# Optimization experiments

Hardware: AMD Instinct MI355X
Metric: run time of the kernel (lower is better)

Reference implementation:

```python
import jax, jax.numpy as jnp
import numpy as np

NUM_GROUPS = 32
EPS = 1e-6

def group_norm(x, gamma, beta):
    B, C, H, W = x.shape
    g = x.reshape(B, NUM_GROUPS, C // NUM_GROUPS, H, W)
    mean = g.mean(axis=(2, 3, 4), keepdims=True)
    var = g.var(axis=(2, 3, 4), keepdims=True)
    g = (g - mean) * jax.lax.rsqrt(var + EPS)
    x = g.reshape(B, C, H, W)
    return x * gamma[None, :, None, None] + beta[None, :, None, None]

def conv1x1(x, w, b):
    # x: [B,C,H,W], w: [Cout,Cin], b: [Cout]
    return jnp.einsum('bchw,oc->bohw', x, w) + b[None, :, None, None]

def setup_inputs() -> dict:
    key = jax.random.key(0)
    ks = jax.random.split(key, 11)
    B, C, H, W = 8, 512, 64, 64
    s = 1.0 / np.sqrt(C)
    return {
        'x': jax.random.normal(ks[0], (B, C, H, W), jnp.float32),
        'gn_w': jnp.ones((C,), jnp.float32),
        'gn_b': jnp.zeros((C,), jnp.float32),
        'q_w': jax.random.normal(ks[1], (C, C), jnp.float32) * s,
        'q_b': jnp.zeros((C,), jnp.float32),
        'k_w': jax.random.normal(ks[2], (C, C), jnp.float32) * s,
        'k_b': jnp.zeros((C,), jnp.float32),
        'v_w': jax.random.normal(ks[3], (C, C), jnp.float32) * s,
        'v_b': jnp.zeros((C,), jnp.float32),
        'proj_w': jax.random.normal(ks[4], (C, C), jnp.float32) * s,
        'proj_b': jnp.zeros((C,), jnp.float32),
    }

def reference(x, gn_w, gn_b, q_w, q_b, k_w, k_b, v_w, v_b, proj_w, proj_b):
    B, C, H, W = x.shape
    h = group_norm(x, gn_w, gn_b)
    q = conv1x1(h, q_w, q_b).reshape(B, C, H * W)  # [B,C,N]
    k = conv1x1(h, k_w, k_b).reshape(B, C, H * W)
    v = conv1x1(h, v_w, v_b).reshape(B, C, H * W)
    # scores: [B, N(query), N(key)]
    w = jnp.einsum('bcn,bcm->bnm', q, k) * (C ** -0.5)
    w = jax.nn.softmax(w, axis=2)
    # out: [B, C, N]
    h = jnp.einsum('bnm,bcm->bcn', w, v).reshape(B, C, H, W)
    return x + conv1x1(h, proj_w, proj_b)
```

## Files before the change

### kernel.cpp

```cpp
#include <hip/hip_runtime.h>
#include <hip/hip_bf16.h>
#include <hip/hip_fp16.h>
#include <stdint.h>


#define C_DIM 512
#define N_DIM 4096
#define CN (512 * 4096)
#define BATCH 8

typedef _Float16 h8 __attribute__((ext_vector_type(8)));
typedef _Float16 h4 __attribute__((ext_vector_type(4)));
typedef float f4 __attribute__((ext_vector_type(4)));

__device__ __forceinline__ void gload16(const void* g, void* l) {
  __builtin_amdgcn_global_load_lds((const __attribute__((address_space(1))) void*)g,
                                   (__attribute__((address_space(3))) void*)l, 16, 0, 0);
}

__device__ __forceinline__ void gemm_core(const _Float16* __restrict__ At, int lda,
                                          const _Float16* __restrict__ Bt, int ldb,
                                          int ksteps, _Float16* lsA, _Float16* lsB,
                                          f4 acc[4][4]) {
  const int t = threadIdx.x, w = t >> 6, lane = t & 63;
  const int rr = lane >> 2, kof = (lane & 3) * 8;
  const _Float16* gA0 = At + (size_t)((w * 2 + 0) * 16 + rr) * lda + kof;
  const _Float16* gA1 = At + (size_t)((w * 2 + 1) * 16 + rr) * lda + kof;
  const _Float16* gB0 = Bt + (size_t)((w * 2 + 0) * 16 + rr) * ldb + kof;
  const _Float16* gB1 = Bt + (size_t)((w * 2 + 1) * 16 + rr) * ldb + kof;
  _Float16* lA0 = lsA + (w * 2 + 0) * 512;
  _Float16* lA1 = lsA + (w * 2 + 1) * 512;
  _Float16* lB0 = lsB + (w * 2 + 0) * 512;
  _Float16* lB1 = lsB + (w * 2 + 1) * 512;
  const int wm = w >> 1, wn = w & 1;
  const int fr = lane & 15, fk = (lane >> 4) * 8;
  for (int ks = 0; ks < ksteps; ++ks) {
    gload16(gA0, lA0);
    gload16(gA1, lA1);
    gload16(gB0, lB0);
    gload16(gB1, lB1);
    __syncthreads();
    h8 af[4], bf[4];
#pragma unroll
    for (int i = 0; i < 4; ++i)
      af[i] = *(const h8*)&lsA[(wm * 64 + i * 16 + fr) * 32 + fk];
#pragma unroll
    for (int j = 0; j < 4; ++j)
      bf[j] = *(const h8*)&lsB[(wn * 64 + j * 16 + fr) * 32 + fk];
#pragma unroll
    for (int i = 0; i < 4; ++i)
#pragma unroll
      for (int j = 0; j < 4; ++j)
        acc[i][j] = __builtin_amdgcn_mfma_f32_16x16x32_f16(af[i], bf[j], acc[i][j], 0, 0, 0);
    __syncthreads();
    gA0 += 32; gA1 += 32; gB0 += 32; gB1 += 32;
  }
}

__device__ __forceinline__ void epi_f16_direct(f4 acc[4][4], _Float16* lsOut,
                                               _Float16* out, int ldo,
                                               const float* bias_tile, float scale) {
  const int t = threadIdx.x, lane = t & 63, w = t >> 6, wm = w >> 1, wn = w & 1;
  const int cr = lane >> 4, cc = lane & 15;
#pragma unroll
  for (int i = 0; i < 4; ++i) {
    const int r0 = wm * 64 + i * 16 + cr * 4;
    float b0 = 0.f, b1 = 0.f, b2 = 0.f, b3 = 0.f;
    if (bias_tile) { b0 = bias_tile[r0]; b1 = bias_tile[r0 + 1];
                     b2 = bias_tile[r0 + 2]; b3 = bias_tile[r0 + 3]; }
#pragma unroll
    for (int j = 0; j < 4; ++j) {
      const int cl = wn * 64 + j * 16 + cc;
      lsOut[(r0 + 0) * 136 + cl] = (_Float16)(acc[i][j].x * scale + b0);
      lsOut[(r0 + 1) * 136 + cl] = (_Float16)(acc[i][j].y * scale + b1);
      lsOut[(r0 + 2) * 136 + cl] = (_Float16)(acc[i][j].z * scale + b2);
      lsOut[(r0 + 3) * 136 + cl] = (_Float16)(acc[i][j].w * scale + b3);
    }
  }
  __syncthreads();
  const int row = t >> 1, co = (t & 1) * 64;
#pragma unroll
  for (int s = 0; s < 8; ++s)
    *(uint4*)(out + (size_t)row * ldo + co + s * 8) =
        *(const uint4*)&lsOut[row * 136 + co + s * 8];
}

__device__ __forceinline__ void epi_f16_trans(f4 acc[4][4], _Float16* lsOut,
                                              _Float16* outT, int ldo,
                                              const float* bias_tile) {
  const int t = threadIdx.x, lane = t & 63, w = t >> 6, wm = w >> 1, wn = w & 1;
  const int cr = lane >> 4, cc = lane & 15;
#pragma unroll
  for (int i = 0; i < 4; ++i) {
    const int r0 = wm * 64 + i * 16 + cr * 4;
    const float b0 = bias_tile[r0], b1 = bias_tile[r0 + 1];
    const float b2 = bias_tile[r0 + 2], b3 = bias_tile[r0 + 3];
#pragma unroll
    for (int j = 0; j < 4; ++j) {
      const int cl = wn * 64 + j * 16 + cc;
      h4 v = {(_Float16)(acc[i][j].x + b0), (_Float16)(acc[i][j].y + b1),
              (_Float16)(acc[i][j].z + b2), (_Float16)(acc[i][j].w + b3)};
      *(h4*)&lsOut[cl * 136 + r0] = v;
    }
  }
  __syncthreads();
  const int row = t >> 1, co = (t & 1) * 64;
#pragma unroll
  for (int s = 0; s < 8; ++s)
    *(uint4*)(outT + (size_t)row * ldo + co + s * 8) =
        *(const uint4*)&lsOut[row * 136 + co + s * 8];
}

__device__ __forceinline__ void epi_f32_direct(f4 acc[4][4], float* out, int ldo,
                                               const float* bias_tile,
                                               const float* resid) {
  const int t = threadIdx.x, lane = t & 63, w = t >> 6, wm = w >> 1, wn = w & 1;
  const int cr = lane >> 4, cc = lane & 15;
#pragma unroll
  for (int i = 0; i < 4; ++i) {
    const int r0 = wm * 64 + i * 16 + cr * 4;
#pragma unroll
    for (int r = 0; r < 4; ++r) {
      const int row = r0 + r;
      const float bv = bias_tile ? bias_tile[row] : 0.f;
#pragma unroll
      for (int j = 0; j < 4; ++j) {
        const int col = wn * 64 + j * 16 + cc;
        float v = acc[i][j][r] + bv;
        if (resid) v += resid[(size_t)row * ldo + col];
        out[(size_t)row * ldo + col] = v;
      }
    }
  }
}

__global__ __launch_bounds__(256) void k_wcvt(const float* __restrict__ w0,
                                              const float* __restrict__ w1,
                                              const float* __restrict__ w2,
                                              const float* __restrict__ w3,
                                              _Float16* __restrict__ out) {
  const int z = blockIdx.y;
  const float* src = z == 0 ? w0 : z == 1 ? w1 : z == 2 ? w2 : w3;
  _Float16* dst = out + (size_t)z * (C_DIM * C_DIM);
  const int idx = (blockIdx.x * 256 + threadIdx.x) * 4;
  f4 v = *(const f4*)(src + idx);
  h4 o = {(_Float16)v.x, (_Float16)v.y, (_Float16)v.z, (_Float16)v.w};
  *(h4*)(dst + idx) = o;
}

__global__ __launch_bounds__(256) void k_gnstats(const float* __restrict__ x,
                                                 float* __restrict__ stats) {
  const int bg = blockIdx.x;
  const f4* x4 = (const f4*)(x + (size_t)bg * (16 * N_DIM));
  const int t = threadIdx.x;
  float s = 0.f, ss = 0.f;
#pragma unroll 4
  for (int i = 0; i < 64; ++i) {
    f4 v = x4[t + i * 256];
    s += v.x + v.y + v.z + v.w;
    ss += v.x * v.x + v.y * v.y + v.z * v.z + v.w * v.w;
  }
  __shared__ float reds[4], redq[4];
  for (int off = 32; off; off >>= 1) {
    s += __shfl_down(s, off);
    ss += __shfl_down(ss, off);
  }
  if ((t & 63) == 0) { reds[t >> 6] = s; redq[t >> 6] = ss; }
  __syncthreads();
  if (t == 0) {
    s = reds[0] + reds[1] + reds[2] + reds[3];
    ss = redq[0] + redq[1] + redq[2] + redq[3];
    const float mean = s * (1.f / (16 * N_DIM));
    const float var = ss * (1.f / (16 * N_DIM)) - mean * mean;
    stats[bg * 2] = mean;
    stats[bg * 2 + 1] = rsqrtf(var + 1e-6f);
  }
}

__global__ __launch_bounds__(256) void k_gnapply(const float* __restrict__ x,
                                                 const float* __restrict__ gw,
                                                 const float* __restrict__ gb,
                                                 const float* __restrict__ stats,
                                                 _Float16* __restrict__ Ht) {
  __shared__ _Float16 lsT[64 * 72];
  const int n0 = blockIdx.x * 64, c0 = blockIdx.y * 64, b = blockIdx.z;
  const int t = threadIdx.x, rc = t >> 2, qc = t & 3;
  const int c = c0 + rc, g = c >> 4;
  const float mean = stats[(b * 32 + g) * 2], rstd = stats[(b * 32 + g) * 2 + 1];
  const float sc = gw[c] * rstd, of = gb[c] - mean * sc;
  const float* xr = x + ((size_t)b * C_DIM + c) * N_DIM + n0;
#pragma unroll
  for (int q = 0; q < 4; ++q) {
    const int f4i = qc + q * 4;
    f4 v = *(const f4*)(xr + f4i * 4);
    const int nl = f4i * 4;
    lsT[(nl + 0) * 72 + rc] = (_Float16)(v.x * sc + of);
    lsT[(nl + 1) * 72 + rc] = (_Float16)(v.y * sc + of);
    lsT[(nl + 2) * 72 + rc] = (_Float16)(v.z * sc + of);
    lsT[(nl + 3) * 72 + rc] = (_Float16)(v.w * sc + of);
  }
  __syncthreads();
  const int j = t >> 2, ch = (t & 3) * 16;
  _Float16* dst = Ht + ((size_t)b * N_DIM + n0 + j) * C_DIM + c0 + ch;
  *(uint4*)dst = *(const uint4*)&lsT[j * 72 + ch];
  *(uint4*)(dst + 8) = *(const uint4*)&lsT[j * 72 + ch + 8];
}

__global__ __launch_bounds__(256) void k_qkv(const _Float16* __restrict__ Wh,
                                             const float* __restrict__ bq,
                                             const float* __restrict__ bk,
                                             const float* __restrict__ bv,
                                             const _Float16* __restrict__ Ht,
                                             _Float16* __restrict__ Qt,
                                             _Float16* __restrict__ Kt,
                                             _Float16* __restrict__ V) {
  __shared__ _Float16 smem[128 * 136];
  const int z = blockIdx.z, b = z / 3, which = z - b * 3;
  const _Float16* A = Wh + (size_t)which * (C_DIM * C_DIM);
  const float* bias = which == 0 ? bq : which == 1 ? bk : bv;
  const int n0 = blockIdx.x * 128, m0 = blockIdx.y * 128;
  f4 acc[4][4] = {};
  gemm_core(A + (size_t)m0 * C_DIM, C_DIM,
            Ht + (size_t)b * CN + (size_t)n0 * C_DIM, C_DIM, 16,
            smem, smem + 4096, acc);
  if (which == 2) {
    epi_f16_direct(acc, smem, V + (size_t)b * CN + (size_t)m0 * N_DIM + n0, N_DIM,
                   bias + m0, 1.f);
  } else {
    _Float16* outT = (which == 0 ? Qt : Kt) + (size_t)b * CN + (size_t)n0 * C_DIM + m0;
    epi_f16_trans(acc, smem, outT, C_DIM, bias + m0);
  }
}

__global__ __launch_bounds__(256) void k_qk(const _Float16* __restrict__ Qt,
                                            const _Float16* __restrict__ Kt,
                                            _Float16* __restrict__ S) {
  __shared__ _Float16 smem[128 * 136];
  const int m0 = blockIdx.x * 128, n0 = blockIdx.y * 128;
  f4 acc[4][4] = {};
  gemm_core(Qt + (size_t)n0 * C_DIM, C_DIM, Kt + (size_t)m0 * C_DIM, C_DIM, 16,
            smem, smem + 4096, acc);
  epi_f16_direct(acc, smem, S + (size_t)n0 * N_DIM + m0, N_DIM, nullptr,
                 0.04419417382415922f);
}

__global__ __launch_bounds__(256) void k_softmax(_Float16* __restrict__ S) {
  _Float16* row = S + (size_t)blockIdx.x * N_DIM;
  const int t = threadIdx.x, lane = t & 63, w = t >> 6;
  _Float16 v[16];
  *(uint4*)&v[0] = *(const uint4*)(row + t * 16);
  *(uint4*)&v[8] = *(const uint4*)(row + t * 16 + 8);
  float f[16], mx = -1e30f;
#pragma unroll
  for (int u = 0; u < 16; ++u) { f[u] = (float)v[u]; mx = fmaxf(mx, f[u]); }
  __shared__ float red[8];
  for (int off = 32; off; off >>= 1) mx = fmaxf(mx, __shfl_down(mx, off));
  if (lane == 0) red[w] = mx;
  __syncthreads();
  mx = fmaxf(fmaxf(red[0], red[1]), fmaxf(red[2], red[3]));
  float sum = 0.f;
#pragma unroll
  for (int u = 0; u < 16; ++u) { f[u] = __expf(f[u] - mx); sum += f[u]; }
  for (int off = 32; off; off >>= 1) sum += __shfl_down(sum, off);
  if (lane == 0) red[4 + w] = sum;
  __syncthreads();
  const float inv = 1.f / (red[4] + red[5] + red[6] + red[7]);
#pragma unroll
  for (int u = 0; u < 16; ++u) v[u] = (_Float16)(f[u] * inv);
  *(uint4*)(row + t * 16) = *(const uint4*)&v[0];
  *(uint4*)(row + t * 16 + 8) = *(const uint4*)&v[8];
}

__global__ __launch_bounds__(256) void k_pv(const _Float16* __restrict__ P,
                                            const _Float16* __restrict__ V,
                                            float* __restrict__ Pp) {
  __shared__ _Float16 smem[2 * 4096];
  const int c0 = blockIdx.x * 128, n0 = blockIdx.y * 128, kz = blockIdx.z;
  f4 acc[4][4] = {};
  gemm_core(P + (size_t)n0 * N_DIM + kz * 1024, N_DIM,
            V + (size_t)c0 * N_DIM + kz * 1024, N_DIM, 32,
            smem, smem + 4096, acc);
  epi_f32_direct(acc, Pp + (size_t)kz * CN + (size_t)n0 * C_DIM + c0, C_DIM,
                 nullptr, nullptr);
}

__global__ __launch_bounds__(256) void k_pvred(const float* __restrict__ Pp,
                                               _Float16* __restrict__ ATTt) {
  const int idx = (blockIdx.x * 256 + threadIdx.x) * 8;
  float a[8];
#pragma unroll
  for (int u = 0; u < 8; ++u) a[u] = 0.f;
#pragma unroll
  for (int kz = 0; kz < 4; ++kz) {
    f4 p0 = *(const f4*)(Pp + (size_t)kz * CN + idx);
    f4 p1 = *(const f4*)(Pp + (size_t)kz * CN + idx + 4);
    a[0] += p0.x; a[1] += p0.y; a[2] += p0.z; a[3] += p0.w;
    a[4] += p1.x; a[5] += p1.y; a[6] += p1.z; a[7] += p1.w;
  }
  h8 o = {(_Float16)a[0], (_Float16)a[1], (_Float16)a[2], (_Float16)a[3],
          (_Float16)a[4], (_Float16)a[5], (_Float16)a[6], (_Float16)a[7]};
  *(h8*)(ATTt + idx) = o;
}

__global__ __launch_bounds__(256) void k_proj(const _Float16* __restrict__ Whp,
                                              const float* __restrict__ bp,
                                              const _Float16* __restrict__ ATTt,
                                              const float* __restrict__ x,
                                              float* __restrict__ out) {
  __shared__ _Float16 smem[2 * 4096];
  const int b = blockIdx.z, n0 = blockIdx.x * 128, m0 = blockIdx.y * 128;
  f4 acc[4][4] = {};
  gemm_core(Whp + (size_t)m0 * C_DIM, C_DIM,
            ATTt + (size_t)b * CN + (size_t)n0 * C_DIM, C_DIM, 16,
            smem, smem + 4096, acc);
  const size_t off = (size_t)b * CN + (size_t)m0 * N_DIM + n0;
  epi_f32_direct(acc, out + off, N_DIM, bp + m0, x + off);
}

extern "C" void kernel_launch(void* const* d_in, const int* in_sizes, int n_in,
                              void* d_out, int out_size, void* d_ws, size_t ws_size,
                              hipStream_t stream) {
  const float* x = (const float*)d_in[0];
  const float* gn_w = (const float*)d_in[1];
  const float* gn_b = (const float*)d_in[2];
  const float* q_w = (const float*)d_in[3];
  const float* q_b = (const float*)d_in[4];
  const float* k_w = (const float*)d_in[5];
  const float* k_b = (const float*)d_in[6];
  const float* v_w = (const float*)d_in[7];
  const float* v_b = (const float*)d_in[8];
  const float* p_w = (const float*)d_in[9];
  const float* p_b = (const float*)d_in[10];
  float* out = (float*)d_out;

  const size_t MB = 1024ull * 1024ull;
  if (ws_size < 164ull * MB) return;
  char* ws = (char*)d_ws;
  _Float16* Wh    = (_Float16*)(ws + 0);
  float*    stats = (float*)(ws + 2 * MB);
  _Float16* Ht    = (_Float16*)(ws + 4 * MB);
  _Float16* Qt    = (_Float16*)(ws + 36 * MB);
  _Float16* Kt    = (_Float16*)(ws + 68 * MB);
  _Float16* V     = (_Float16*)(ws + 100 * MB);
  float*    Pp    = (float*)(ws + 132 * MB);
  _Float16* S     = Ht;
  _Float16* ATTt  = Qt;

  k_wcvt<<<dim3(256, 4), 256, 0, stream>>>(q_w, k_w, v_w, p_w, Wh);
  k_gnstats<<<dim3(256), 256, 0, stream>>>(x, stats);
  k_gnapply<<<dim3(64, 8, 8), 256, 0, stream>>>(x, gn_w, gn_b, stats, Ht);
  k_qkv<<<dim3(32, 4, 24), 256, 0, stream>>>(Wh, q_b, k_b, v_b, Ht, Qt, Kt, V);
  for (int b = 0; b < BATCH; ++b) {
    k_qk<<<dim3(32, 32), 256, 0, stream>>>(Qt + (size_t)b * CN, Kt + (size_t)b * CN, S);
    k_softmax<<<dim3(4096), 256, 0, stream>>>(S);
    k_pv<<<dim3(4, 32, 4), 256, 0, stream>>>(S, V + (size_t)b * CN, Pp);
    k_pvred<<<dim3(1024), 256, 0, stream>>>(Pp, ATTt + (size_t)b * CN);
  }
  k_proj<<<dim3(32, 4, 8), 256, 0, stream>>>(Wh + 3 * C_DIM * C_DIM, p_b, ATTt, x, out);
}
```

Baseline: 987.8 us.

## Batch attention over several images per launch and drop split-K PV reduction

```diff
diff --git a/kernel.cpp b/kernel.cpp
--- a/kernel.cpp
+++ b/kernel.cpp
@@ -7,6 +7,7 @@
 #define C_DIM 512
 #define N_DIM 4096
 #define CN (512 * 4096)
+#define NN ((size_t)4096 * 4096)
 #define BATCH 8
 
 typedef _Float16 h8 __attribute__((ext_vector_type(8)));
@@ -236,16 +237,17 @@
                                             const _Float16* __restrict__ Kt,
                                             _Float16* __restrict__ S) {
   __shared__ _Float16 smem[128 * 136];
-  const int m0 = blockIdx.x * 128, n0 = blockIdx.y * 128;
+  const int m0 = blockIdx.x * 128, n0 = blockIdx.y * 128, bz = blockIdx.z;
   f4 acc[4][4] = {};
-  gemm_core(Qt + (size_t)n0 * C_DIM, C_DIM, Kt + (size_t)m0 * C_DIM, C_DIM, 16,
+  gemm_core(Qt + (size_t)bz * CN + (size_t)n0 * C_DIM, C_DIM,
+            Kt + (size_t)bz * CN + (size_t)m0 * C_DIM, C_DIM, 16,
             smem, smem + 4096, acc);
-  epi_f16_direct(acc, smem, S + (size_t)n0 * N_DIM + m0, N_DIM, nullptr,
-                 0.04419417382415922f);
+  epi_f16_direct(acc, smem, S + (size_t)bz * NN + (size_t)n0 * N_DIM + m0, N_DIM,
+                 nullptr, 0.04419417382415922f);
 }
 
 __global__ __launch_bounds__(256) void k_softmax(_Float16* __restrict__ S) {
-  _Float16* row = S + (size_t)blockIdx.x * N_DIM;
+  _Float16* row = S + (size_t)blockIdx.y * NN + (size_t)blockIdx.x * N_DIM;
   const int t = threadIdx.x, lane = t & 63, w = t >> 6;
   _Float16 v[16];
   *(uint4*)&v[0] = *(const uint4*)(row + t * 16);
@@ -271,35 +273,17 @@
   *(uint4*)(row + t * 16 + 8) = *(const uint4*)&v[8];
 }
 
-__global__ __launch_bounds__(256) void k_pv(const _Float16* __restrict__ P,
+__global__ __launch_bounds__(256) void k_pv(const _Float16* __restrict__ S,
                                             const _Float16* __restrict__ V,
-                                            float* __restrict__ Pp) {
-  __shared__ _Float16 smem[2 * 4096];
-  const int c0 = blockIdx.x * 128, n0 = blockIdx.y * 128, kz = blockIdx.z;
+                                            _Float16* __restrict__ ATTt) {
+  __shared__ _Float16 smem[128 * 136];
+  const int c0 = blockIdx.x * 128, n0 = blockIdx.y * 128, bz = blockIdx.z;
   f4 acc[4][4] = {};
-  gemm_core(P + (size_t)n0 * N_DIM + kz * 1024, N_DIM,
-            V + (size_t)c0 * N_DIM + kz * 1024, N_DIM, 32,
+  gemm_core(S + (size_t)bz * NN + (size_t)n0 * N_DIM, N_DIM,
+            V + (size_t)bz * CN + (size_t)c0 * N_DIM, N_DIM, 128,
             smem, smem + 4096, acc);
-  epi_f32_direct(acc, Pp + (size_t)kz * CN + (size_t)n0 * C_DIM + c0, C_DIM,
-                 nullptr, nullptr);
-}
-
-__global__ __launch_bounds__(256) void k_pvred(const float* __restrict__ Pp,
-                                               _Float16* __restrict__ ATTt) {
-  const int idx = (blockIdx.x * 256 + threadIdx.x) * 8;
-  float a[8];
-#pragma unroll
-  for (int u = 0; u < 8; ++u) a[u] = 0.f;
-#pragma unroll
-  for (int kz = 0; kz < 4; ++kz) {
-    f4 p0 = *(const f4*)(Pp + (size_t)kz * CN + idx);
-    f4 p1 = *(const f4*)(Pp + (size_t)kz * CN + idx + 4);
-    a[0] += p0.x; a[1] += p0.y; a[2] += p0.z; a[3] += p0.w;
-    a[4] += p1.x; a[5] += p1.y; a[6] += p1.z; a[7] += p1.w;
-  }
-  h8 o = {(_Float16)a[0], (_Float16)a[1], (_Float16)a[2], (_Float16)a[3],
-          (_Float16)a[4], (_Float16)a[5], (_Float16)a[6], (_Float16)a[7]};
-  *(h8*)(ATTt + idx) = o;
+  epi_f16_direct(acc, smem, ATTt + (size_t)bz * CN + (size_t)n0 * C_DIM + c0, C_DIM,
+                 nullptr, 1.f);
 }
 
 __global__ __launch_bounds__(256) void k_proj(const _Float16* __restrict__ Whp,
@@ -307,7 +291,7 @@
                                               const _Float16* __restrict__ ATTt,
                                               const float* __restrict__ x,
                                               float* __restrict__ out) {
-  __shared__ _Float16 smem[2 * 4096];
+  __shared__ _Float16 smem[128 * 136];
   const int b = blockIdx.z, n0 = blockIdx.x * 128, m0 = blockIdx.y * 128;
   f4 acc[4][4] = {};
   gemm_core(Whp + (size_t)m0 * C_DIM, C_DIM,
@@ -323,38 +307,37 @@
   const float* x = (const float*)d_in[0];
   const float* gn_w = (const float*)d_in[1];
   const float* gn_b = (const float*)d_in[2];
-  const float* q_w = (const float*)d_in[3];
   const float* q_b = (const float*)d_in[4];
-  const float* k_w = (const float*)d_in[5];
   const float* k_b = (const float*)d_in[6];
-  const float* v_w = (const float*)d_in[7];
   const float* v_b = (const float*)d_in[8];
-  const float* p_w = (const float*)d_in[9];
   const float* p_b = (const float*)d_in[10];
   float* out = (float*)d_out;
 
   const size_t MB = 1024ull * 1024ull;
   if (ws_size < 164ull * MB) return;
+  const int G = (ws_size >= 388ull * MB) ? 8
+              : (ws_size >= 260ull * MB) ? 4
+              : (ws_size >= 196ull * MB) ? 2 : 1;
+
   char* ws = (char*)d_ws;
   _Float16* Wh    = (_Float16*)(ws + 0);
   float*    stats = (float*)(ws + 2 * MB);
-  _Float16* Ht    = (_Float16*)(ws + 4 * MB);
-  _Float16* Qt    = (_Float16*)(ws + 36 * MB);
-  _Float16* Kt    = (_Float16*)(ws + 68 * MB);
-  _Float16* V     = (_Float16*)(ws + 100 * MB);
-  float*    Pp    = (float*)(ws + 132 * MB);
+  _Float16* Qt    = (_Float16*)(ws + 4 * MB);
+  _Float16* Kt    = (_Float16*)(ws + 36 * MB);
+  _Float16* V     = (_Float16*)(ws + 68 * MB);
+  _Float16* ATTt  = (_Float16*)(ws + 100 * MB);
+  _Float16* Ht    = (_Float16*)(ws + 132 * MB);
   _Float16* S     = Ht;
-  _Float16* ATTt  = Qt;
-
-  k_wcvt<<<dim3(256, 4), 256, 0, stream>>>(q_w, k_w, v_w, p_w, Wh);
+
+  k_wcvt<<<dim3(256, 4), 256, 0, stream>>>((const float*)d_in[3], (const float*)d_in[5],
+                                           (const float*)d_in[7], (const float*)d_in[9], Wh);
   k_gnstats<<<dim3(256), 256, 0, stream>>>(x, stats);
   k_gnapply<<<dim3(64, 8, 8), 256, 0, stream>>>(x, gn_w, gn_b, stats, Ht);
   k_qkv<<<dim3(32, 4, 24), 256, 0, stream>>>(Wh, q_b, k_b, v_b, Ht, Qt, Kt, V);
-  for (int b = 0; b < BATCH; ++b) {
-    k_qk<<<dim3(32, 32), 256, 0, stream>>>(Qt + (size_t)b * CN, Kt + (size_t)b * CN, S);
-    k_softmax<<<dim3(4096), 256, 0, stream>>>(S);
-    k_pv<<<dim3(4, 32, 4), 256, 0, stream>>>(S, V + (size_t)b * CN, Pp);
-    k_pvred<<<dim3(1024), 256, 0, stream>>>(Pp, ATTt + (size_t)b * CN);
+  for (int g = 0; g < BATCH; g += G) {
+    k_qk<<<dim3(32, 32, G), 256, 0, stream>>>(Qt + (size_t)g * CN, Kt + (size_t)g * CN, S);
+    k_softmax<<<dim3(4096, G), 256, 0, stream>>>(S);
+    k_pv<<<dim3(4, 32, G), 256, 0, stream>>>(S, V + (size_t)g * CN, ATTt + (size_t)g * CN);
   }
   k_proj<<<dim3(32, 4, 8), 256, 0, stream>>>(Wh + 3 * C_DIM * C_DIM, p_b, ATTt, x, out);
 }
```

Measured after the change: 971.3 us. About the same (-1.7%).
